# Performance work log

Hardware: AMD Instinct MI355X
Metric: run time of the kernel (lower is better)

Reference implementation:

```python
import jax, jax.numpy as jnp
import numpy as np

G, N, E, B = 4, 100000, 500000, 512
V, D, H, C = 50000, 300, 128, 20
NUM_HEADS, STEPS = 3, 2


def setup_inputs() -> dict:
    key = jax.random.key(0)
    ks = jax.random.split(key, 12)
    return {
        "node_indices": jax.random.randint(ks[0], (G, N), 0, V),
        "src": jax.random.randint(ks[1], (G, E), 0, N),
        "dst": jax.random.randint(ks[2], (G, E), 0, N),
        "node_graph_ids": jnp.sort(jax.random.randint(ks[3], (G, N), 0, B), axis=-1),
        "edge_weights": jax.random.uniform(ks[4], (G, E), dtype=jnp.float32),
        "emb_table": jax.random.normal(ks[5], (V, D), dtype=jnp.float32) * 0.1,
        "edge_params": jnp.ones((G,), dtype=jnp.float32),
        "W_proj": jax.random.normal(ks[6], (G, D, H), dtype=jnp.float32) / np.sqrt(D),
        "b_proj": jnp.zeros((G, H), dtype=jnp.float32),
        "W_cls": jax.random.normal(ks[7], (G, H, C), dtype=jnp.float32) / np.sqrt(H),
        "b_cls": jnp.zeros((G, C), dtype=jnp.float32),
        "W_fuse": jax.random.normal(ks[8], (NUM_HEADS, C, C, G), dtype=jnp.float32) / np.sqrt(C * G),
        "b_fuse": jnp.zeros((NUM_HEADS, C), dtype=jnp.float32),
    }


def _per_graph_logits(idx, s, d, gid, ew, emb_table, ep, Wp, bp, Wc, bc):
    # embedding lookup + input projection: [N, H]
    h = emb_table[idx] @ Wp + bp
    # graph_learning: relu(scalar * edge_weights)
    w = jax.nn.relu(ep * ew)  # [E]
    # in-degree for DGL mean reduce (0 in-edges -> 0 agg)
    deg = jax.ops.segment_sum(jnp.ones_like(ew), d, num_segments=N)
    inv_deg = jnp.where(deg > 0, 1.0 / deg, 0.0)[:, None]  # [N, 1]
    for _ in range(STEPS):
        msg = h[s] * w[:, None]                                   # gather-multiply [E, H]
        agg = jax.ops.segment_sum(msg, d, num_segments=N) * inv_deg  # scatter-mean [N, H]
        h = h + agg
    # dgl.mean_nodes: per-document mean of node features
    cnt = jax.ops.segment_sum(jnp.ones((N,), h.dtype), gid, num_segments=B)
    doc = jax.ops.segment_sum(h, gid, num_segments=B) / jnp.maximum(cnt, 1.0)[:, None]  # [B, H]
    # classify (dropout = identity in eval)
    return jax.nn.relu(doc) @ Wc + bc  # [B, C]


def reference(node_indices, src, dst, node_graph_ids, edge_weights, emb_table,
              edge_params, W_proj, b_proj, W_cls, b_cls, W_fuse, b_fuse):
    per_graph = jax.vmap(_per_graph_logits,
                         in_axes=(0, 0, 0, 0, 0, None, 0, 0, 0, 0, 0))
    logits = per_graph(node_indices, src, dst, node_graph_ids, edge_weights,
                       emb_table, edge_params, W_proj, b_proj, W_cls, b_cls)  # [G, B, C]
    stacked = jnp.transpose(logits, (1, 2, 0))  # [B, C_in, G] (Conv1d input, kernel=G)
    # Conv1d(out=C, in=C, k=G) per head, valid -> length 1, squeezed
    head_out = jnp.einsum('big,hoig->hbo', stacked, W_fuse) + b_fuse[:, None, :]  # [NH, B, C]
    fused_logits = head_out.mean(axis=0)  # [B, C]
    predictions = jax.nn.softmax(fused_logits, axis=-1)
    return predictions, fused_logits
```

## Files before the change

kernel.cpp:

```cpp
#include <hip/hip_runtime.h>

#define G_  4
#define N_  100000
#define E_  500000
#define B_  512
#define V_  50000
#define D_  300
#define H_  128
#define C_  20
#define NH_ 3

#define KP_  320
#define SCB_  512
#define NBLK_ ((N_ + SCB_ - 1) / SCB_)

typedef unsigned short ushort_t;
typedef __attribute__((ext_vector_type(8))) short bf16x8;
typedef __attribute__((ext_vector_type(4))) float f32x4;

__device__ __forceinline__ ushort_t f2bf(float f) {
    unsigned int x = __float_as_uint(f);
    unsigned int r = x + 0x7FFFu + ((x >> 16) & 1u);
    return (ushort_t)(r >> 16);
}

__device__ __forceinline__ int lower_bound_i(const int* __restrict__ a, int n, int v) {
    int lo = 0, hi = n;
    while (lo < hi) {
        int mid = (lo + hi) >> 1;
        if (a[mid] < v) lo = mid + 1; else hi = mid;
    }
    return lo;
}

__device__ __forceinline__ void unpack8(uint4 u, float* f) {
    f[0] = __uint_as_float((u.x & 0xFFFFu) << 16);
    f[1] = __uint_as_float(u.x & 0xFFFF0000u);
    f[2] = __uint_as_float((u.y & 0xFFFFu) << 16);
    f[3] = __uint_as_float(u.y & 0xFFFF0000u);
    f[4] = __uint_as_float((u.z & 0xFFFFu) << 16);
    f[5] = __uint_as_float(u.z & 0xFFFF0000u);
    f[6] = __uint_as_float((u.w & 0xFFFFu) << 16);
    f[7] = __uint_as_float(u.w & 0xFFFF0000u);
}

__global__ __launch_bounds__(256) void convert_w_kernel(
    const float* __restrict__ Wp,
    ushort_t* __restrict__ Wt)
{
    int flat = blockIdx.x * 256 + threadIdx.x;
    int g = flat / (H_ * KP_);
    int r = flat % (H_ * KP_);
    int n = r / KP_;
    int k = r % KP_;
    float v = (k < D_) ? Wp[((size_t)g * D_ + k) * H_ + n] : 0.f;
    Wt[flat] = f2bf(v);
}

template <int NG>
__global__ __launch_bounds__(256) void mfma_gemm_lds_kernel(
    const float* __restrict__ emb,
    const ushort_t* __restrict__ Wt,
    const float* __restrict__ bp,
    ushort_t* __restrict__ Ph)
{
    __shared__ float As[32][36];

    const int t    = threadIdx.x;
    const int w    = t >> 6;
    const int l    = t & 63;
    const int l16  = l & 15;
    const int lk   = (l >> 4) * 8;
    const int ch   = w * 32;
    const int rowbase = blockIdx.x * 32;

    const int srow = t >> 3;
    const int skq  = t & 7;
    const int grow = min(rowbase + srow, V_ - 1);
    const float* arow_p = &emb[(size_t)grow * D_];

    auto ldA = [&](int k0) -> float4 {
        int k = k0 + skq * 4;
        if (k + 4 <= D_) return *reinterpret_cast<const float4*>(arow_p + k);
        float4 v = make_float4(0.f, 0.f, 0.f, 0.f);
        if (k     < D_) v.x = arow_p[k];
        if (k + 1 < D_) v.y = arow_p[k + 1];
        if (k + 2 < D_) v.z = arow_p[k + 2];
        if (k + 3 < D_) v.w = arow_p[k + 3];
        return v;
    };

    f32x4 acc[NG][2][2];
#pragma unroll
    for (int g = 0; g < NG; ++g)
#pragma unroll
        for (int m = 0; m < 2; ++m)
#pragma unroll
            for (int n = 0; n < 2; ++n) acc[g][m][n] = (f32x4){0.f, 0.f, 0.f, 0.f};

    float4 pf = ldA(0);

    for (int k0 = 0; k0 < KP_; k0 += 32) {
        As[srow][skq * 4 + 0] = pf.x;
        As[srow][skq * 4 + 1] = pf.y;
        As[srow][skq * 4 + 2] = pf.z;
        As[srow][skq * 4 + 3] = pf.w;
        __syncthreads();

        if (k0 + 32 < KP_) pf = ldA(k0 + 32);

        bf16x8 a[2];
#pragma unroll
        for (int m = 0; m < 2; ++m) {
            const float* ap = &As[m * 16 + l16][lk];
            float4 x0 = *reinterpret_cast<const float4*>(ap);
            float4 x1 = *reinterpret_cast<const float4*>(ap + 4);
            a[m][0] = (short)f2bf(x0.x); a[m][1] = (short)f2bf(x0.y);
            a[m][2] = (short)f2bf(x0.z); a[m][3] = (short)f2bf(x0.w);
            a[m][4] = (short)f2bf(x1.x); a[m][5] = (short)f2bf(x1.y);
            a[m][6] = (short)f2bf(x1.z); a[m][7] = (short)f2bf(x1.w);
        }

        const int kb = k0 + lk;
#pragma unroll
        for (int g = 0; g < NG; ++g) {
            const ushort_t* Wg = Wt + (size_t)g * H_ * KP_;
            bf16x8 b[2];
#pragma unroll
            for (int n = 0; n < 2; ++n)
                b[n] = *reinterpret_cast<const bf16x8*>(
                    &Wg[(size_t)(ch + n * 16 + l16) * KP_ + kb]);
#pragma unroll
            for (int m = 0; m < 2; ++m)
#pragma unroll
                for (int n = 0; n < 2; ++n)
                    acc[g][m][n] = __builtin_amdgcn_mfma_f32_16x16x32_bf16(
                        a[m], b[n], acc[g][m][n], 0, 0, 0);
        }
        __syncthreads();
    }

    const int rbase = (l >> 4) * 4;
#pragma unroll
    for (int g = 0; g < NG; ++g) {
        ushort_t* Pg = Ph + (size_t)g * V_ * H_;
#pragma unroll
        for (int n = 0; n < 2; ++n) {
            const int col  = ch + n * 16 + l16;
            const float bv = bp[g * H_ + col];
#pragma unroll
            for (int m = 0; m < 2; ++m) {
#pragma unroll
                for (int r = 0; r < 4; ++r) {
                    int row = rowbase + m * 16 + rbase + r;
                    if (row < V_)
                        Pg[(size_t)row * H_ + col] = f2bf(acc[g][m][n][r] + bv);
                }
            }
        }
    }
}

__global__ __launch_bounds__(256) void deg_count_kernel(const int* __restrict__ dstA,
                                                        int* __restrict__ deg)
{
    const int g = blockIdx.y;
    int e = blockIdx.x * 256 + threadIdx.x;
    if (e < E_) atomicAdd(&deg[g * N_ + dstA[(size_t)g * E_ + e]], 1);
}

__global__ __launch_bounds__(512) void scan1_kernel(const int* __restrict__ deg,
                                                    int* __restrict__ bsum)
{
    __shared__ int sh[512];
    const int g = blockIdx.y, b = blockIdx.x, t = threadIdx.x;
    int i = b * SCB_ + t;
    sh[t] = (i < N_) ? deg[g * N_ + i] : 0;
    __syncthreads();
#pragma unroll
    for (int ofs = 256; ofs > 0; ofs >>= 1) {
        if (t < ofs) sh[t] += sh[t + ofs];
        __syncthreads();
    }
    if (t == 0) bsum[g * NBLK_ + b] = sh[0];
}

__global__ __launch_bounds__(256) void scan2_kernel(const int* __restrict__ bsum,
                                                    int* __restrict__ bpre,
                                                    int* __restrict__ off)
{
    __shared__ int sh[256];
    const int g = blockIdx.x, t = threadIdx.x;
    int v = (t < NBLK_) ? bsum[g * NBLK_ + t] : 0;
    sh[t] = v;
    __syncthreads();
#pragma unroll
    for (int ofs = 1; ofs < 256; ofs <<= 1) {
        int u = (t >= ofs) ? sh[t - ofs] : 0;
        __syncthreads();
        sh[t] += u;
        __syncthreads();
    }
    if (t < NBLK_) bpre[g * (NBLK_ + 1) + t + 1] = sh[t];
    if (t == 0) {
        bpre[g * (NBLK_ + 1)] = 0;
        off[(size_t)g * (N_ + 1) + N_] = sh[NBLK_ - 1];
    }
}

__global__ __launch_bounds__(512) void scan3_kernel(int* __restrict__ deg,
                                                    const int* __restrict__ bpre,
                                                    int* __restrict__ off)
{
    __shared__ int sh[512];
    const int g = blockIdx.y, b = blockIdx.x, t = threadIdx.x;
    int i = b * SCB_ + t;
    int v = (i < N_) ? deg[g * N_ + i] : 0;
    sh[t] = v;
    __syncthreads();
#pragma unroll
    for (int ofs = 1; ofs < 512; ofs <<= 1) {
        int u = (t >= ofs) ? sh[t - ofs] : 0;
        __syncthreads();
        sh[t] += u;
        __syncthreads();
    }
    if (i < N_) {
        off[(size_t)g * (N_ + 1) + i] = bpre[g * (NBLK_ + 1) + b] + sh[t] - v;
        deg[g * N_ + i] = 0;
    }
}

__global__ __launch_bounds__(256) void scatter_kernel(
    const int* __restrict__ srcA, const int* __restrict__ dstA,
    const float* __restrict__ ewA, const float* __restrict__ ep,
    const int* __restrict__ idxA, const int* __restrict__ off,
    int* __restrict__ cnt, int4* __restrict__ csr4)
{
    const int g = blockIdx.y;
    int e = blockIdx.x * 256 + threadIdx.x;
    if (e >= E_) return;
    int s = srcA[(size_t)g * E_ + e];
    int d = dstA[(size_t)g * E_ + e];
    int pos = off[(size_t)g * (N_ + 1) + d] + atomicAdd(&cnt[g * N_ + d], 1);
    float w = ep[g] * ewA[(size_t)g * E_ + e];
    csr4[(size_t)g * E_ + pos] =
        make_int4(s, idxA[(size_t)g * N_ + s], __float_as_int(fmaxf(w, 0.f)), 0);
}

__global__ __launch_bounds__(256) void prop1_kernel(
    const int* __restrict__ idx_g, const int* __restrict__ off,
    const int4* __restrict__ csr4,
    const ushort_t* __restrict__ Ph, ushort_t* __restrict__ hBh)
{
    const int n = blockIdx.x * 16 + (threadIdx.x >> 4);
    if (n >= N_) return;
    const int lane = threadIdx.x & 15;
    const int col  = lane * 8;

    const int lo = off[n], hi = off[n + 1];

    float sf[8];
    unpack8(*reinterpret_cast<const uint4*>(&Ph[(size_t)idx_g[n] * H_ + col]), sf);

    float acc[8];
#pragma unroll
    for (int j = 0; j < 8; ++j) acc[j] = 0.f;

    int i = lo;
    for (; i + 4 <= hi; i += 4) {
        int4 e0 = csr4[i],     e1 = csr4[i + 1];
        int4 e2 = csr4[i + 2], e3 = csr4[i + 3];
        float c0 = __int_as_float(e0.z), c1 = __int_as_float(e1.z);
        float c2 = __int_as_float(e2.z), c3 = __int_as_float(e3.z);
        uint4 u0 = *reinterpret_cast<const uint4*>(&Ph[(size_t)e0.y * H_ + col]);
        uint4 u1 = *reinterpret_cast<const uint4*>(&Ph[(size_t)e1.y * H_ + col]);
        uint4 u2 = *reinterpret_cast<const uint4*>(&Ph[(size_t)e2.y * H_ + col]);
        uint4 u3 = *reinterpret_cast<const uint4*>(&Ph[(size_t)e3.y * H_ + col]);
        float f0[8], f1[8], f2[8], f3[8];
        unpack8(u0, f0); unpack8(u1, f1); unpack8(u2, f2); unpack8(u3, f3);
#pragma unroll
        for (int j = 0; j < 8; ++j)
            acc[j] += c0 * f0[j] + c1 * f1[j] + c2 * f2[j] + c3 * f3[j];
    }
    for (; i < hi; ++i) {
        int4 e0 = csr4[i];
        float c = __int_as_float(e0.z);
        float f[8];
        unpack8(*reinterpret_cast<const uint4*>(&Ph[(size_t)e0.y * H_ + col]), f);
#pragma unroll
        for (int j = 0; j < 8; ++j) acc[j] += c * f[j];
    }

    const float inv = (hi > lo) ? 1.0f / (float)(hi - lo) : 0.f;
    ushort_t p[8];
#pragma unroll
    for (int j = 0; j < 8; ++j) p[j] = f2bf(sf[j] + inv * acc[j]);
    uint4 o;
    o.x = (unsigned)p[0] | ((unsigned)p[1] << 16);
    o.y = (unsigned)p[2] | ((unsigned)p[3] << 16);
    o.z = (unsigned)p[4] | ((unsigned)p[5] << 16);
    o.w = (unsigned)p[6] | ((unsigned)p[7] << 16);
    *reinterpret_cast<uint4*>(&hBh[(size_t)n * H_ + col]) = o;
}

__global__ __launch_bounds__(256) void prop2_fused_kernel(
    const int* __restrict__ off, const int4* __restrict__ csr4,
    const int* __restrict__ gid,
    const ushort_t* __restrict__ hBh, float* __restrict__ docsum)
{
    const int nloc = threadIdx.x >> 4;
    const int n    = blockIdx.x * 16 + nloc;
    const int lane = threadIdx.x & 15;
    const int col  = lane * 8;

    __shared__ float sh[16][H_];
    __shared__ int   shgid[16];

    float o[8];
    if (n < N_) {
        const int lo = off[n], hi = off[n + 1];

        float sf[8];
        unpack8(*reinterpret_cast<const uint4*>(&hBh[(size_t)n * H_ + col]), sf);

        float acc[8];
#pragma unroll
        for (int j = 0; j < 8; ++j) acc[j] = 0.f;

        int i = lo;
        for (; i + 4 <= hi; i += 4) {
            int4 e0 = csr4[i],     e1 = csr4[i + 1];
            int4 e2 = csr4[i + 2], e3 = csr4[i + 3];
            float c0 = __int_as_float(e0.z), c1 = __int_as_float(e1.z);
            float c2 = __int_as_float(e2.z), c3 = __int_as_float(e3.z);
            uint4 u0 = *reinterpret_cast<const uint4*>(&hBh[(size_t)e0.x * H_ + col]);
            uint4 u1 = *reinterpret_cast<const uint4*>(&hBh[(size_t)e1.x * H_ + col]);
            uint4 u2 = *reinterpret_cast<const uint4*>(&hBh[(size_t)e2.x * H_ + col]);
            uint4 u3 = *reinterpret_cast<const uint4*>(&hBh[(size_t)e3.x * H_ + col]);
            float f0[8], f1[8], f2[8], f3[8];
            unpack8(u0, f0); unpack8(u1, f1); unpack8(u2, f2); unpack8(u3, f3);
#pragma unroll
            for (int j = 0; j < 8; ++j)
                acc[j] += c0 * f0[j] + c1 * f1[j] + c2 * f2[j] + c3 * f3[j];
        }
        for (; i < hi; ++i) {
            int4 e0 = csr4[i];
            float c = __int_as_float(e0.z);
            float f[8];
            unpack8(*reinterpret_cast<const uint4*>(&hBh[(size_t)e0.x * H_ + col]), f);
#pragma unroll
            for (int j = 0; j < 8; ++j) acc[j] += c * f[j];
        }

        const float inv = (hi > lo) ? 1.0f / (float)(hi - lo) : 0.f;
#pragma unroll
        for (int j = 0; j < 8; ++j) o[j] = sf[j] + inv * acc[j];
        if (lane == 0) shgid[nloc] = gid[n];
    } else {
#pragma unroll
        for (int j = 0; j < 8; ++j) o[j] = 0.f;
        if (lane == 0) shgid[nloc] = -1;
    }

#pragma unroll
    for (int j = 0; j < 8; ++j) sh[nloc][col + j] = o[j];
    __syncthreads();

    const int c  = threadIdx.x & 127;
    const int q  = threadIdx.x >> 7;
    const int n0 = q * 8;
    float run = 0.f;
    int rgid = shgid[n0];
    for (int k = 0; k < 8; ++k) {
        int gk = shgid[n0 + k];
        if (gk != rgid) {
            if (rgid >= 0) atomicAdd(&docsum[(size_t)rgid * H_ + c], run);
            run = 0.f; rgid = gk;
        }
        run += sh[n0 + k][c];
    }
    if (rgid >= 0) atomicAdd(&docsum[(size_t)rgid * H_ + c], run);
}

__global__ __launch_bounds__(128) void cls_kernel(
    const int* __restrict__ gidA, const float* __restrict__ docsum,
    const float* __restrict__ Wc, const float* __restrict__ bc,
    float* __restrict__ logits)
{
    const int b   = blockIdx.x;
    const int g   = blockIdx.y;
    const int tid = threadIdx.x;
    const int* gid = gidA + (size_t)g * N_;

    int lo = lower_bound_i(gid, N_, b);
    int hi = lower_bound_i(gid, N_, b + 1);
    float cnt = (float)(hi - lo);

    __shared__ float sdoc[H_];
    float dv = docsum[((size_t)g * B_ + b) * H_ + tid] / fmaxf(cnt, 1.0f);
    sdoc[tid] = fmaxf(dv, 0.f);
    __syncthreads();

    if (tid < C_) {
        const float* Wcg = Wc + (size_t)g * H_ * C_;
        float acc = bc[g * C_ + tid];
#pragma unroll 8
        for (int hh = 0; hh < H_; ++hh) acc += sdoc[hh] * Wcg[hh * C_ + tid];
        logits[((size_t)g * B_ + b) * C_ + tid] = acc;
    }
}

__global__ __launch_bounds__(64) void fuse_kernel(
    const float* __restrict__ logits,
    const float* __restrict__ Wf,
    const float* __restrict__ bf,
    float* __restrict__ out)
{
    const int b   = blockIdx.x;
    const int tid = threadIdx.x;

    __shared__ float s[C_ * G_];
    __shared__ float fl[C_];

    for (int t = tid; t < C_ * G_; t += 64) {
        int i = t >> 2, g = t & 3;
        s[t] = logits[((long)g * B_ + b) * C_ + i];
    }
    __syncthreads();

    if (tid < C_) {
        float acc = 0.f;
        for (int hd = 0; hd < NH_; ++hd) {
            float a = bf[hd * C_ + tid];
            const float* wrow = &Wf[((hd * C_ + tid) * C_) * G_];
#pragma unroll 5
        for (int i = 0; i < C_; ++i) {
#pragma unroll
                for (int g = 0; g < G_; ++g)
                    a += s[i * G_ + g] * wrow[i * G_ + g];
            }
            acc += a;
        }
        fl[tid] = acc * (1.0f / 3.0f);
    }
    __syncthreads();

    if (tid < C_) {
        float f = fl[tid];
        float m = -1e30f;
#pragma unroll
        for (int i = 0; i < C_; ++i) m = fmaxf(m, fl[i]);
        float ssum = 0.f;
#pragma unroll
        for (int i = 0; i < C_; ++i) ssum += expf(fl[i] - m);
        out[b * C_ + tid] = expf(f - m) / ssum;
        out[B_ * C_ + b * C_ + tid] = f;
    }
}

extern "C" void kernel_launch(void* const* d_in, const int* in_sizes, int n_in,
                              void* d_out, int out_size, void* d_ws, size_t ws_size,
                              hipStream_t stream)
{
    const int*   node_indices = (const int*)d_in[0];
    const int*   srcA         = (const int*)d_in[1];
    const int*   dstA         = (const int*)d_in[2];
    const int*   gidA         = (const int*)d_in[3];
    const float* ewA          = (const float*)d_in[4];
    const float* emb          = (const float*)d_in[5];
    const float* ep           = (const float*)d_in[6];
    const float* Wp           = (const float*)d_in[7];
    const float* bp           = (const float*)d_in[8];
    const float* Wc           = (const float*)d_in[9];
    const float* bc           = (const float*)d_in[10];
    const float* Wf           = (const float*)d_in[11];
    const float* bf           = (const float*)d_in[12];
    float*       out          = (float*)d_out;

    char* wp0 = (char*)d_ws;
    auto alloc = [&](size_t bytes) {
        void* r = (void*)wp0;
        wp0 += (bytes + 255) & ~(size_t)255;
        return r;
    };
    ushort_t* hBh      = (ushort_t*)alloc((size_t)N_ * H_ * 2);
    float*    docsum   = (float*)   alloc((size_t)G_ * B_ * H_ * 4);
    float*    logits   = (float*)   alloc((size_t)G_ * B_ * C_ * 4);
    ushort_t* Wt       = (ushort_t*)alloc((size_t)G_ * H_ * KP_ * 2);
    int*      deg_i    = (int*)     alloc((size_t)G_ * N_ * 4);
    int*      off      = (int*)     alloc((size_t)G_ * (N_ + 1) * 4);
    int*      bsum     = (int*)     alloc((size_t)G_ * NBLK_ * 4);
    int*      bpre     = (int*)     alloc((size_t)G_ * (NBLK_ + 1) * 4);
    int4*     csr4     = (int4*)    alloc((size_t)G_ * E_ * 16);

    const size_t pbytes = (size_t)V_ * H_ * 2;
    size_t used  = (size_t)(wp0 - (char*)d_ws);
    size_t avail = (ws_size > used) ? ws_size - used : 0;

    int ng;
    if (avail >= 4 * pbytes + 1024)      ng = 4;
    else if (avail >= 2 * pbytes + 1024) ng = 2;
    else                                 ng = 1;
    ushort_t* Ph = (ushort_t*)alloc((size_t)ng * pbytes);

    convert_w_kernel<<<(G_ * H_ * KP_) / 256, 256, 0, stream>>>(Wp, Wt);
    hipMemsetAsync(docsum, 0, (size_t)G_ * B_ * H_ * sizeof(float), stream);

    hipMemsetAsync(deg_i, 0, (size_t)G_ * N_ * sizeof(int), stream);
    deg_count_kernel<<<dim3((E_ + 255) / 256, G_), 256, 0, stream>>>(dstA, deg_i);
    scan1_kernel<<<dim3(NBLK_, G_), 512, 0, stream>>>(deg_i, bsum);
    scan2_kernel<<<G_, 256, 0, stream>>>(bsum, bpre, off);
    scan3_kernel<<<dim3(NBLK_, G_), 512, 0, stream>>>(deg_i, bpre, off);
    scatter_kernel<<<dim3((E_ + 255) / 256, G_), 256, 0, stream>>>(
        srcA, dstA, ewA, ep, node_indices, off, deg_i, csr4);

    const int gemm_blocks = (V_ + 31) / 32;
    for (int gbase = 0; gbase < G_; gbase += ng) {
        const ushort_t* Wtg = Wt + (size_t)gbase * H_ * KP_;
        const float*    bpg = bp + (size_t)gbase * H_;
        if (ng == 4)
            mfma_gemm_lds_kernel<4><<<gemm_blocks, 256, 0, stream>>>(emb, Wtg, bpg, Ph);
        else if (ng == 2)
            mfma_gemm_lds_kernel<2><<<gemm_blocks, 256, 0, stream>>>(emb, Wtg, bpg, Ph);
        else
            mfma_gemm_lds_kernel<1><<<gemm_blocks, 256, 0, stream>>>(emb, Wtg, bpg, Ph);

        for (int gi = 0; gi < ng; ++gi) {
            const int g = gbase + gi;
            const int*      idx   = node_indices + (size_t)g * N_;
            const int*      gid   = gidA + (size_t)g * N_;
            const int*      off_g = off + (size_t)g * (N_ + 1);
            const int4*     csr_g = csr4 + (size_t)g * E_;
            const ushort_t* Pg    = Ph + (size_t)gi * V_ * H_;

            prop1_kernel<<<(N_ + 15) / 16, 256, 0, stream>>>(
                idx, off_g, csr_g, Pg, hBh);
            prop2_fused_kernel<<<(N_ + 15) / 16, 256, 0, stream>>>(
                off_g, csr_g, gid, hBh, docsum + (size_t)g * B_ * H_);
        }
    }

    cls_kernel<<<dim3(B_, G_), 128, 0, stream>>>(gidA, docsum, Wc, bc, logits);
    fuse_kernel<<<B_, 64, 0, stream>>>(logits, Wf, bf, out);
}
```

Measured before the change: 533.6 us.

## Pre-convert embeddings to bf16 and shrink CSR entries to int2

Adds a kernel that converts the embedding table to padded bf16 once, so the projection GEMM loads half the bytes and no longer converts fp32 to bf16 inside its inner loop. The CSR records shrink from int4 (src, idx, weight, pad) to int2 (edge id, idx). The propagation kernels now look up edge weight and source node indirectly through the edge id. This halves CSR bandwidth but adds scattered loads of ew and src per edge in the prop kernels.

```diff
diff --git a/kernel.cpp b/kernel.cpp
--- a/kernel.cpp
+++ b/kernel.cpp
@@ -57,14 +57,35 @@
     Wt[flat] = f2bf(v);
 }
 
+__global__ __launch_bounds__(256) void convert_emb_kernel(
+    const float* __restrict__ emb,
+    ushort_t* __restrict__ embh)
+{
+    int flat = blockIdx.x * 256 + threadIdx.x;
+    if (flat >= V_ * (KP_ / 8)) return;
+    int v = flat / (KP_ / 8);
+    int k = (flat % (KP_ / 8)) * 8;
+    const float* src = &emb[(size_t)v * D_ + k];
+    ushort_t p[8];
+#pragma unroll
+    for (int j = 0; j < 8; ++j)
+        p[j] = (k + j < D_) ? f2bf(src[j]) : (ushort_t)0;
+    uint4 o;
+    o.x = (unsigned)p[0] | ((unsigned)p[1] << 16);
+    o.y = (unsigned)p[2] | ((unsigned)p[3] << 16);
+    o.z = (unsigned)p[4] | ((unsigned)p[5] << 16);
+    o.w = (unsigned)p[6] | ((unsigned)p[7] << 16);
+    *reinterpret_cast<uint4*>(&embh[(size_t)v * KP_ + k]) = o;
+}
+
 template <int NG>
 __global__ __launch_bounds__(256) void mfma_gemm_lds_kernel(
-    const float* __restrict__ emb,
+    const ushort_t* __restrict__ embh,
     const ushort_t* __restrict__ Wt,
     const float* __restrict__ bp,
     ushort_t* __restrict__ Ph)
 {
-    __shared__ float As[32][36];
+    __shared__ ushort_t As[32][40];
 
     const int t    = threadIdx.x;
     const int w    = t >> 6;
@@ -77,18 +98,7 @@
     const int srow = t >> 3;
     const int skq  = t & 7;
     const int grow = min(rowbase + srow, V_ - 1);
-    const float* arow_p = &emb[(size_t)grow * D_];
-
-    auto ldA = [&](int k0) -> float4 {
-        int k = k0 + skq * 4;
-        if (k + 4 <= D_) return *reinterpret_cast<const float4*>(arow_p + k);
-        float4 v = make_float4(0.f, 0.f, 0.f, 0.f);
-        if (k     < D_) v.x = arow_p[k];
-        if (k + 1 < D_) v.y = arow_p[k + 1];
-        if (k + 2 < D_) v.z = arow_p[k + 2];
-        if (k + 3 < D_) v.w = arow_p[k + 3];
-        return v;
-    };
+    const ushort_t* arow_p = &embh[(size_t)grow * KP_];
 
     f32x4 acc[NG][2][2];
 #pragma unroll
@@ -98,28 +108,19 @@
 #pragma unroll
             for (int n = 0; n < 2; ++n) acc[g][m][n] = (f32x4){0.f, 0.f, 0.f, 0.f};
 
-    float4 pf = ldA(0);
+    uint2 pf = *reinterpret_cast<const uint2*>(arow_p + skq * 4);
 
     for (int k0 = 0; k0 < KP_; k0 += 32) {
-        As[srow][skq * 4 + 0] = pf.x;
-        As[srow][skq * 4 + 1] = pf.y;
-        As[srow][skq * 4 + 2] = pf.z;
-        As[srow][skq * 4 + 3] = pf.w;
-        __syncthreads();
-
-        if (k0 + 32 < KP_) pf = ldA(k0 + 32);
+        *reinterpret_cast<uint2*>(&As[srow][skq * 4]) = pf;
+        __syncthreads();
+
+        if (k0 + 32 < KP_)
+            pf = *reinterpret_cast<const uint2*>(arow_p + k0 + 32 + skq * 4);
 
         bf16x8 a[2];
 #pragma unroll
-        for (int m = 0; m < 2; ++m) {
-            const float* ap = &As[m * 16 + l16][lk];
-            float4 x0 = *reinterpret_cast<const float4*>(ap);
-            float4 x1 = *reinterpret_cast<const float4*>(ap + 4);
-            a[m][0] = (short)f2bf(x0.x); a[m][1] = (short)f2bf(x0.y);
-            a[m][2] = (short)f2bf(x0.z); a[m][3] = (short)f2bf(x0.w);
-            a[m][4] = (short)f2bf(x1.x); a[m][5] = (short)f2bf(x1.y);
-            a[m][6] = (short)f2bf(x1.z); a[m][7] = (short)f2bf(x1.w);
-        }
+        for (int m = 0; m < 2; ++m)
+            a[m] = *reinterpret_cast<const bf16x8*>(&As[m * 16 + l16][lk]);
 
         const int kb = k0 + lk;
 #pragma unroll
@@ -233,9 +234,8 @@
 
 __global__ __launch_bounds__(256) void scatter_kernel(
     const int* __restrict__ srcA, const int* __restrict__ dstA,
-    const float* __restrict__ ewA, const float* __restrict__ ep,
     const int* __restrict__ idxA, const int* __restrict__ off,
-    int* __restrict__ cnt, int4* __restrict__ csr4)
+    int* __restrict__ cnt, int2* __restrict__ csr2)
 {
     const int g = blockIdx.y;
     int e = blockIdx.x * 256 + threadIdx.x;
@@ -243,20 +243,20 @@
     int s = srcA[(size_t)g * E_ + e];
     int d = dstA[(size_t)g * E_ + e];
     int pos = off[(size_t)g * (N_ + 1) + d] + atomicAdd(&cnt[g * N_ + d], 1);
-    float w = ep[g] * ewA[(size_t)g * E_ + e];
-    csr4[(size_t)g * E_ + pos] =
-        make_int4(s, idxA[(size_t)g * N_ + s], __float_as_int(fmaxf(w, 0.f)), 0);
+    csr2[(size_t)g * E_ + pos] = make_int2(e, idxA[(size_t)g * N_ + s]);
 }
 
 __global__ __launch_bounds__(256) void prop1_kernel(
     const int* __restrict__ idx_g, const int* __restrict__ off,
-    const int4* __restrict__ csr4,
+    const int2* __restrict__ csr2, const float* __restrict__ ew,
+    const float* __restrict__ ep,
     const ushort_t* __restrict__ Ph, ushort_t* __restrict__ hBh)
 {
     const int n = blockIdx.x * 16 + (threadIdx.x >> 4);
     if (n >= N_) return;
     const int lane = threadIdx.x & 15;
     const int col  = lane * 8;
+    const float ep0 = ep[0];
 
     const int lo = off[n], hi = off[n + 1];
 
@@ -269,10 +269,12 @@
 
     int i = lo;
     for (; i + 4 <= hi; i += 4) {
-        int4 e0 = csr4[i],     e1 = csr4[i + 1];
-        int4 e2 = csr4[i + 2], e3 = csr4[i + 3];
-        float c0 = __int_as_float(e0.z), c1 = __int_as_float(e1.z);
-        float c2 = __int_as_float(e2.z), c3 = __int_as_float(e3.z);
+        int2 e0 = csr2[i],     e1 = csr2[i + 1];
+        int2 e2 = csr2[i + 2], e3 = csr2[i + 3];
+        float c0 = fmaxf(ep0 * ew[e0.x], 0.f);
+        float c1 = fmaxf(ep0 * ew[e1.x], 0.f);
+        float c2 = fmaxf(ep0 * ew[e2.x], 0.f);
+        float c3 = fmaxf(ep0 * ew[e3.x], 0.f);
         uint4 u0 = *reinterpret_cast<const uint4*>(&Ph[(size_t)e0.y * H_ + col]);
         uint4 u1 = *reinterpret_cast<const uint4*>(&Ph[(size_t)e1.y * H_ + col]);
         uint4 u2 = *reinterpret_cast<const uint4*>(&Ph[(size_t)e2.y * H_ + col]);
@@ -284,8 +286,8 @@
             acc[j] += c0 * f0[j] + c1 * f1[j] + c2 * f2[j] + c3 * f3[j];
     }
     for (; i < hi; ++i) {
-        int4 e0 = csr4[i];
-        float c = __int_as_float(e0.z);
+        int2 e0 = csr2[i];
+        float c = fmaxf(ep0 * ew[e0.x], 0.f);
         float f[8];
         unpack8(*reinterpret_cast<const uint4*>(&Ph[(size_t)e0.y * H_ + col]), f);
 #pragma unroll
@@ -305,14 +307,16 @@
 }
 
 __global__ __launch_bounds__(256) void prop2_fused_kernel(
-    const int* __restrict__ off, const int4* __restrict__ csr4,
-    const int* __restrict__ gid,
+    const int* __restrict__ off, const int2* __restrict__ csr2,
+    const int* __restrict__ src, const float* __restrict__ ew,
+    const float* __restrict__ ep, const int* __restrict__ gid,
     const ushort_t* __restrict__ hBh, float* __restrict__ docsum)
 {
     const int nloc = threadIdx.x >> 4;
     const int n    = blockIdx.x * 16 + nloc;
     const int lane = threadIdx.x & 15;
     const int col  = lane * 8;
+    const float ep0 = ep[0];
 
     __shared__ float sh[16][H_];
     __shared__ int   shgid[16];
@@ -330,14 +334,17 @@
 
         int i = lo;
         for (; i + 4 <= hi; i += 4) {
-            int4 e0 = csr4[i],     e1 = csr4[i + 1];
-            int4 e2 = csr4[i + 2], e3 = csr4[i + 3];
-            float c0 = __int_as_float(e0.z), c1 = __int_as_float(e1.z);
-            float c2 = __int_as_float(e2.z), c3 = __int_as_float(e3.z);
-            uint4 u0 = *reinterpret_cast<const uint4*>(&hBh[(size_t)e0.x * H_ + col]);
-            uint4 u1 = *reinterpret_cast<const uint4*>(&hBh[(size_t)e1.x * H_ + col]);
-            uint4 u2 = *reinterpret_cast<const uint4*>(&hBh[(size_t)e2.x * H_ + col]);
-            uint4 u3 = *reinterpret_cast<const uint4*>(&hBh[(size_t)e3.x * H_ + col]);
+            int2 e0 = csr2[i],     e1 = csr2[i + 1];
+            int2 e2 = csr2[i + 2], e3 = csr2[i + 3];
+            int s0 = src[e0.x], s1 = src[e1.x], s2 = src[e2.x], s3 = src[e3.x];
+            float c0 = fmaxf(ep0 * ew[e0.x], 0.f);
+            float c1 = fmaxf(ep0 * ew[e1.x], 0.f);
+            float c2 = fmaxf(ep0 * ew[e2.x], 0.f);
+            float c3 = fmaxf(ep0 * ew[e3.x], 0.f);
+            uint4 u0 = *reinterpret_cast<const uint4*>(&hBh[(size_t)s0 * H_ + col]);
+            uint4 u1 = *reinterpret_cast<const uint4*>(&hBh[(size_t)s1 * H_ + col]);
+            uint4 u2 = *reinterpret_cast<const uint4*>(&hBh[(size_t)s2 * H_ + col]);
+            uint4 u3 = *reinterpret_cast<const uint4*>(&hBh[(size_t)s3 * H_ + col]);
             float f0[8], f1[8], f2[8], f3[8];
             unpack8(u0, f0); unpack8(u1, f1); unpack8(u2, f2); unpack8(u3, f3);
 #pragma unroll
@@ -345,10 +352,11 @@
                 acc[j] += c0 * f0[j] + c1 * f1[j] + c2 * f2[j] + c3 * f3[j];
         }
         for (; i < hi; ++i) {
-            int4 e0 = csr4[i];
-            float c = __int_as_float(e0.z);
+            int2 e0 = csr2[i];
+            int s = src[e0.x];
+            float c = fmaxf(ep0 * ew[e0.x], 0.f);
             float f[8];
-            unpack8(*reinterpret_cast<const uint4*>(&hBh[(size_t)e0.x * H_ + col]), f);
+            unpack8(*reinterpret_cast<const uint4*>(&hBh[(size_t)s * H_ + col]), f);
 #pragma unroll
             for (int j = 0; j < 8; ++j) acc[j] += c * f[j];
         }
@@ -435,7 +443,7 @@
             float a = bf[hd * C_ + tid];
             const float* wrow = &Wf[((hd * C_ + tid) * C_) * G_];
 #pragma unroll 5
-        for (int i = 0; i < C_; ++i) {
+            for (int i = 0; i < C_; ++i) {
 #pragma unroll
                 for (int g = 0; g < G_; ++g)
                     a += s[i * G_ + g] * wrow[i * G_ + g];
@@ -485,6 +493,7 @@
         return r;
     };
     ushort_t* hBh      = (ushort_t*)alloc((size_t)N_ * H_ * 2);
+    ushort_t* embh     = (ushort_t*)alloc((size_t)V_ * KP_ * 2);
     float*    docsum   = (float*)   alloc((size_t)G_ * B_ * H_ * 4);
     float*    logits   = (float*)   alloc((size_t)G_ * B_ * C_ * 4);
     ushort_t* Wt       = (ushort_t*)alloc((size_t)G_ * H_ * KP_ * 2);
@@ -492,7 +501,7 @@
     int*      off      = (int*)     alloc((size_t)G_ * (N_ + 1) * 4);
     int*      bsum     = (int*)     alloc((size_t)G_ * NBLK_ * 4);
     int*      bpre     = (int*)     alloc((size_t)G_ * (NBLK_ + 1) * 4);
-    int4*     csr4     = (int4*)    alloc((size_t)G_ * E_ * 16);
+    int2*     csr2     = (int2*)    alloc((size_t)G_ * E_ * 8);
 
     const size_t pbytes = (size_t)V_ * H_ * 2;
     size_t used  = (size_t)(wp0 - (char*)d_ws);
@@ -505,6 +514,7 @@
     ushort_t* Ph = (ushort_t*)alloc((size_t)ng * pbytes);
 
     convert_w_kernel<<<(G_ * H_ * KP_) / 256, 256, 0, stream>>>(Wp, Wt);
+    convert_emb_kernel<<<(V_ * (KP_ / 8) + 255) / 256, 256, 0, stream>>>(emb, embh);
     hipMemsetAsync(docsum, 0, (size_t)G_ * B_ * H_ * sizeof(float), stream);
 
     hipMemsetAsync(deg_i, 0, (size_t)G_ * N_ * sizeof(int), stream);
@@ -513,31 +523,34 @@
     scan2_kernel<<<G_, 256, 0, stream>>>(bsum, bpre, off);
     scan3_kernel<<<dim3(NBLK_, G_), 512, 0, stream>>>(deg_i, bpre, off);
     scatter_kernel<<<dim3((E_ + 255) / 256, G_), 256, 0, stream>>>(
-        srcA, dstA, ewA, ep, node_indices, off, deg_i, csr4);
+        srcA, dstA, node_indices, off, deg_i, csr2);
 
     const int gemm_blocks = (V_ + 31) / 32;
     for (int gbase = 0; gbase < G_; gbase += ng) {
         const ushort_t* Wtg = Wt + (size_t)gbase * H_ * KP_;
         const float*    bpg = bp + (size_t)gbase * H_;
         if (ng == 4)
-            mfma_gemm_lds_kernel<4><<<gemm_blocks, 256, 0, stream>>>(emb, Wtg, bpg, Ph);
+            mfma_gemm_lds_kernel<4><<<gemm_blocks, 256, 0, stream>>>(embh, Wtg, bpg, Ph);
         else if (ng == 2)
-            mfma_gemm_lds_kernel<2><<<gemm_blocks, 256, 0, stream>>>(emb, Wtg, bpg, Ph);
+            mfma_gemm_lds_kernel<2><<<gemm_blocks, 256, 0, stream>>>(embh, Wtg, bpg, Ph);
         else
-            mfma_gemm_lds_kernel<1><<<gemm_blocks, 256, 0, stream>>>(emb, Wtg, bpg, Ph);
+            mfma_gemm_lds_kernel<1><<<gemm_blocks, 256, 0, stream>>>(embh, Wtg, bpg, Ph);
 
         for (int gi = 0; gi < ng; ++gi) {
             const int g = gbase + gi;
             const int*      idx   = node_indices + (size_t)g * N_;
             const int*      gid   = gidA + (size_t)g * N_;
             const int*      off_g = off + (size_t)g * (N_ + 1);
-            const int4*     csr_g = csr4 + (size_t)g * E_;
+            const int2*     csr_g = csr2 + (size_t)g * E_;
+            const float*    ew_g  = ewA + (size_t)g * E_;
+            const int*      src_g = srcA + (size_t)g * E_;
             const ushort_t* Pg    = Ph + (size_t)gi * V_ * H_;
 
             prop1_kernel<<<(N_ + 15) / 16, 256, 0, stream>>>(
-                idx, off_g, csr_g, Pg, hBh);
+                idx, off_g, csr_g, ew_g, ep + g, Pg, hBh);
             prop2_fused_kernel<<<(N_ + 15) / 16, 256, 0, stream>>>(
-                off_g, csr_g, gid, hBh, docsum + (size_t)g * B_ * H_);
+                off_g, csr_g, src_g, ew_g, ep + g, gid, hBh,
+                docsum + (size_t)g * B_ * H_);
         }
     }
 
```

New measurement: 618.9 us. +16.0%, slower.

## Load full embedding tile into LDS via async global_load_lds with XOR swizzle

Applied to the files above, without the earlier changes.

The projection GEMM now fetches the block's whole 32x320 fp32 embedding tile up front with global_load_lds (direct global-to-LDS DMA), instead of staging it 32 columns at a time through registers. This leaves one barrier instead of a pair per k-step. An XOR swizzle on 16-byte chunks is meant to avoid LDS bank conflicts on the fragment reads. LDS use per block grows to 40 KB, which may lower occupancy, and the padded k columns past 300 get real data from column 0 instead of zeros.

```diff
diff --git a/kernel.cpp b/kernel.cpp
--- a/kernel.cpp
+++ b/kernel.cpp
@@ -14,6 +14,9 @@
 #define SCB_  512
 #define NBLK_ ((N_ + SCB_ - 1) / SCB_)
 
+#define AROWS_  32
+#define APITCH_ 320
+
 typedef unsigned short ushort_t;
 typedef __attribute__((ext_vector_type(8))) short bf16x8;
 typedef __attribute__((ext_vector_type(4))) float f32x4;
@@ -58,13 +61,13 @@
 }
 
 template <int NG>
-__global__ __launch_bounds__(256) void mfma_gemm_lds_kernel(
+__global__ __launch_bounds__(256) void mfma_gemm_async_kernel(
     const float* __restrict__ emb,
     const ushort_t* __restrict__ Wt,
     const float* __restrict__ bp,
     ushort_t* __restrict__ Ph)
 {
-    __shared__ float As[32][36];
+    __shared__ float As[AROWS_ * APITCH_];
 
     const int t    = threadIdx.x;
     const int w    = t >> 6;
@@ -72,23 +75,26 @@
     const int l16  = l & 15;
     const int lk   = (l >> 4) * 8;
     const int ch   = w * 32;
-    const int rowbase = blockIdx.x * 32;
-
-    const int srow = t >> 3;
-    const int skq  = t & 7;
-    const int grow = min(rowbase + srow, V_ - 1);
-    const float* arow_p = &emb[(size_t)grow * D_];
-
-    auto ldA = [&](int k0) -> float4 {
-        int k = k0 + skq * 4;
-        if (k + 4 <= D_) return *reinterpret_cast<const float4*>(arow_p + k);
-        float4 v = make_float4(0.f, 0.f, 0.f, 0.f);
-        if (k     < D_) v.x = arow_p[k];
-        if (k + 1 < D_) v.y = arow_p[k + 1];
-        if (k + 2 < D_) v.z = arow_p[k + 2];
-        if (k + 3 < D_) v.w = arow_p[k + 3];
-        return v;
-    };
+    const int rowbase = blockIdx.x * AROWS_;
+
+#pragma unroll
+    for (int j = 0; j < 10; ++j) {
+        const int call      = w * 10 + j;
+        const int flat_byte = call * 1024 + l * 16;
+        const int r         = flat_byte / 1280;
+        const int q_sw      = (flat_byte - r * 1280) >> 4;
+        int q_un = q_sw ^ (r & 7);
+        int koff = q_un << 4;
+        if (koff >= 1200) koff = 0;
+        int grow = rowbase + r;
+        if (grow > V_ - 1) grow = V_ - 1;
+        const float* gsrc = emb + (size_t)grow * D_ + (koff >> 2);
+        __builtin_amdgcn_global_load_lds(
+            (const __attribute__((address_space(1))) void*)gsrc,
+            (__attribute__((address_space(3))) void*)(As + call * 256),
+            16, 0, 0);
+    }
+    __syncthreads();
 
     f32x4 acc[NG][2][2];
 #pragma unroll
@@ -98,23 +104,20 @@
 #pragma unroll
             for (int n = 0; n < 2; ++n) acc[g][m][n] = (f32x4){0.f, 0.f, 0.f, 0.f};
 
-    float4 pf = ldA(0);
-
-    for (int k0 = 0; k0 < KP_; k0 += 32) {
-        As[srow][skq * 4 + 0] = pf.x;
-        As[srow][skq * 4 + 1] = pf.y;
-        As[srow][skq * 4 + 2] = pf.z;
-        As[srow][skq * 4 + 3] = pf.w;
-        __syncthreads();
-
-        if (k0 + 32 < KP_) pf = ldA(k0 + 32);
+#pragma unroll
+    for (int k0i = 0; k0i < 10; ++k0i) {
+        const int k0 = k0i * 32;
 
         bf16x8 a[2];
 #pragma unroll
         for (int m = 0; m < 2; ++m) {
-            const float* ap = &As[m * 16 + l16][lk];
-            float4 x0 = *reinterpret_cast<const float4*>(ap);
-            float4 x1 = *reinterpret_cast<const float4*>(ap + 4);
+            const int r  = m * 16 + l16;
+            const int q0 = (k0 + lk) >> 2;
+            const int s  = r & 7;
+            float4 x0 = *reinterpret_cast<const float4*>(
+                &As[r * APITCH_ + ((q0 ^ s) << 2)]);
+            float4 x1 = *reinterpret_cast<const float4*>(
+                &As[r * APITCH_ + (((q0 + 1) ^ s) << 2)]);
             a[m][0] = (short)f2bf(x0.x); a[m][1] = (short)f2bf(x0.y);
             a[m][2] = (short)f2bf(x0.z); a[m][3] = (short)f2bf(x0.w);
             a[m][4] = (short)f2bf(x1.x); a[m][5] = (short)f2bf(x1.y);
@@ -137,7 +140,6 @@
                     acc[g][m][n] = __builtin_amdgcn_mfma_f32_16x16x32_bf16(
                         a[m], b[n], acc[g][m][n], 0, 0, 0);
         }
-        __syncthreads();
     }
 
     const int rbase = (l >> 4) * 4;
@@ -435,7 +437,7 @@
             float a = bf[hd * C_ + tid];
             const float* wrow = &Wf[((hd * C_ + tid) * C_) * G_];
 #pragma unroll 5
-        for (int i = 0; i < C_; ++i) {
+            for (int i = 0; i < C_; ++i) {
 #pragma unroll
                 for (int g = 0; g < G_; ++g)
                     a += s[i * G_ + g] * wrow[i * G_ + g];
@@ -515,16 +517,16 @@
     scatter_kernel<<<dim3((E_ + 255) / 256, G_), 256, 0, stream>>>(
         srcA, dstA, ewA, ep, node_indices, off, deg_i, csr4);
 
-    const int gemm_blocks = (V_ + 31) / 32;
+    const int gemm_blocks = (V_ + AROWS_ - 1) / AROWS_;
     for (int gbase = 0; gbase < G_; gbase += ng) {
         const ushort_t* Wtg = Wt + (size_t)gbase * H_ * KP_;
         const float*    bpg = bp + (size_t)gbase * H_;
         if (ng == 4)
-            mfma_gemm_lds_kernel<4><<<gemm_blocks, 256, 0, stream>>>(emb, Wtg, bpg, Ph);
+            mfma_gemm_async_kernel<4><<<gemm_blocks, 256, 0, stream>>>(emb, Wtg, bpg, Ph);
         else if (ng == 2)
-            mfma_gemm_lds_kernel<2><<<gemm_blocks, 256, 0, stream>>>(emb, Wtg, bpg, Ph);
+            mfma_gemm_async_kernel<2><<<gemm_blocks, 256, 0, stream>>>(emb, Wtg, bpg, Ph);
         else
-            mfma_gemm_lds_kernel<1><<<gemm_blocks, 256, 0, stream>>>(emb, Wtg, bpg, Ph);
+            mfma_gemm_async_kernel<1><<<gemm_blocks, 256, 0, stream>>>(emb, Wtg, bpg, Ph);
 
         for (int gi = 0; gi < ng; ++gi) {
             const int g = gbase + gi;
```

Measured after the change: 530.5 us. No clear change (-0.6%).
